# Performance work log

Hardware: AMD Instinct MI355X
Metric: run time of the kernel (lower is better)

## Reference

```python
import jax, jax.numpy as jnp
import numpy as np

N, F_IN, F_OUT = 2048, 128, 64


def setup_inputs() -> dict:
    key = jax.random.key(0)
    k0, k1, k2, k3, k4 = jax.random.split(key, 5)
    node_features = jax.random.normal(k0, (N, F_IN), dtype=jnp.float32)
    adjacency_matrix = jax.random.uniform(k1, (N, N), dtype=jnp.float32)
    mask_father = jax.random.uniform(k2, (N, N), dtype=jnp.float32)
    mask_hadamard = jax.random.uniform(k3, (N, N), dtype=jnp.float32)
    # kaiming_uniform (fan_in, relu): bound = sqrt(6 / fan_in) * sqrt(2) adjustment -> gain*sqrt(3/fan_in)
    bound = np.sqrt(2.0) * np.sqrt(3.0 / F_IN)
    weight = jax.random.uniform(k4, (F_IN, F_OUT), dtype=jnp.float32, minval=-bound, maxval=bound)
    bias = jnp.zeros((F_OUT,), dtype=jnp.float32)
    return {
        "node_features": node_features,
        "adjacency_matrix": adjacency_matrix,
        "mask_father": mask_father,
        "mask_hadamard": mask_hadamard,
        "weight": weight,
        "bias": bias,
    }


def reference(node_features, adjacency_matrix, mask_father, mask_hadamard, weight, bias):
    # H[i,f] = (X @ W + b)[i,f]
    H = node_features @ weight + bias  # [N, F]
    # Original math: out[j,f] = sum_k mf[j,k] * H[k,f] * (sum_i A[j,i] * H[i,f] * mh[i,k])
    # G[j,f,k] corresponds to the (masked hadamard @ adjacency) intermediate [N, F, N]
    G = jnp.einsum('ji,if,ik->jfk', adjacency_matrix, H, mask_hadamard)
    out = jnp.einsum('jfk,kf,jk->jf', G, H, mask_father)
    return out
```

## Files before the change

### kernel.cpp

```cpp
#include <hip/hip_runtime.h>
#include <hip/hip_bf16.h>


typedef __attribute__((ext_vector_type(8))) _Float16 f16x8;
typedef __attribute__((ext_vector_type(4))) _Float16 f16x4;
typedef __attribute__((ext_vector_type(4))) float f32x4;

#define N 2048
#define FOUT 64
#define FIN 128
#define BI 64
#define NIT 512

__device__ __forceinline__ void gl_lds16(const _Float16* g, _Float16* l) {
    __builtin_amdgcn_global_load_lds(
        (const __attribute__((address_space(1))) void*)g,
        (__attribute__((address_space(3))) void*)l, 16, 0, 0);
}


__global__ __launch_bounds__(256) void k_h(const float* __restrict__ X,
                                           const float* __restrict__ W,
                                           const float* __restrict__ bias,
                                           float* __restrict__ HT,
                                           _Float16* __restrict__ HTh) {
    __shared__ float Ws[FIN * FOUT];
    __shared__ float Xs[4 * FIN];
    int t = threadIdx.x;
#pragma unroll
    for (int s = 0; s < 32; ++s) Ws[t + 256 * s] = W[t + 256 * s];
    int i0 = blockIdx.x * 4;
#pragma unroll
    for (int s = 0; s < 2; ++s) { int idx = t + 256 * s; Xs[idx] = X[(size_t)i0 * FIN + idx]; }
    __syncthreads();
    int f = t & 63, il = t >> 6;
    float h = bias[f];
#pragma unroll
    for (int p = 0; p < FIN; ++p) h = fmaf(Xs[il * FIN + p], Ws[p * FOUT + f], h);
    int i = i0 + il;
    HT[f * N + i] = h;
    HTh[f * N + i] = (_Float16)h;
}

__global__ __launch_bounds__(256) void k_a2h(const float* __restrict__ A,
                                             _Float16* __restrict__ Ah) {
    int g = blockIdx.x * 256 + threadIdx.x;
    float4 v = ((const float4*)A)[g];
    f16x4 o;
    o[0] = (_Float16)v.x; o[1] = (_Float16)v.y; o[2] = (_Float16)v.z; o[3] = (_Float16)v.w;
    ((f16x4*)Ah)[g] = o;
}

__global__ __launch_bounds__(256) void k_mht(const float* __restrict__ mh,
                                             _Float16* __restrict__ mhT) {
    __shared__ float tile[64][65];
    int t = threadIdx.x;
    int bx = blockIdx.x & 31;
    int by = blockIdx.x >> 5;
#pragma unroll
    for (int s = 0; s < 16; ++s) {
        int lin = t + 256 * s;
        int r = lin >> 6, c = lin & 63;
        tile[r][c] = mh[(size_t)(by * 64 + r) * N + bx * 64 + c];
    }
    __syncthreads();
#pragma unroll
    for (int s = 0; s < 16; ++s) {
        int lin = t + 256 * s;
        int kr = lin >> 6, ic = lin & 63;
        mhT[(size_t)(bx * 64 + kr) * N + by * 64 + ic] = (_Float16)tile[ic][kr];
    }
}

__global__ __launch_bounds__(256, 2) void k_main(const float* __restrict__ mf,
                                                 const float* __restrict__ HT,
                                                 const _Float16* __restrict__ HTh,
                                                 const _Float16* __restrict__ Ah,
                                                 const _Float16* __restrict__ mhT,
                                                 float* __restrict__ out) {
    __shared__ _Float16 tiles[2][2][128 * BI];
    __shared__ _Float16 hbuf[2][N];
    __shared__ float red[2][4][64];

    int t = threadIdx.x;
    int jbase = (blockIdx.x >> 5) << 7;
    int f0 = (blockIdx.x & 31) << 1;
    int w = t >> 6, lane = t & 63, q = lane >> 4, l16 = lane & 15;
    int wj = (w & 1) << 6, wk = (w >> 1) << 6;

#pragma unroll
    for (int s = 0; s < 2; ++s) {
        int idx = t + 256 * s;
        ((f16x8*)hbuf)[idx] = *(const f16x8*)&HTh[(size_t)(f0 + (idx >> 8)) * N + (idx & 255) * 8];
    }

    int lrow = lane >> 3;
    int lchunk = (lane & 7) ^ lrow;
    int a_base = (jbase + w * 32 + lrow) * N + lchunk * 8;
    int b_base = (w * 32 + lrow) * N + lchunk * 8;
    int lds_w = w * 2048;

    float outp[2][4][4];
#pragma unroll
    for (int fi = 0; fi < 2; ++fi)
#pragma unroll
        for (int a = 0; a < 4; ++a)
#pragma unroll
            for (int b = 0; b < 4; ++b) outp[fi][a][b] = 0.f;

    {
        const _Float16* pa = Ah + a_base;
        const _Float16* pb = mhT + b_base;
        _Float16* la = &tiles[0][0][lds_w];
        _Float16* lb = &tiles[0][1][lds_w];
#pragma unroll
        for (int c = 0; c < 4; ++c) {
            gl_lds16(pa + c * 8 * N, la + c * 512);
            gl_lds16(pb + c * 8 * N, lb + c * 512);
        }
    }

    f32x4 acc[2][4][4];
#pragma unroll
    for (int fi = 0; fi < 2; ++fi)
#pragma unroll
        for (int a = 0; a < 4; ++a)
#pragma unroll
            for (int b = 0; b < 4; ++b) acc[fi][a][b] = (f32x4){0.f, 0.f, 0.f, 0.f};

    for (int it = 0; it < NIT; ++it) {
        int buf = it & 1;
        int ibase = (it & 31) << 6;
        int kbase = (it >> 5) << 7;

        __syncthreads();

        if (it + 1 < NIT) {
            int ib2 = ((it + 1) & 31) << 6;
            int kt2 = (it + 1) >> 5;
            const _Float16* pa = Ah + a_base + ib2;
            const _Float16* pb = mhT + b_base + kt2 * 128 * N + ib2;
            _Float16* la = &tiles[buf ^ 1][0][lds_w];
            _Float16* lb = &tiles[buf ^ 1][1][lds_w];
#pragma unroll
            for (int c = 0; c < 4; ++c) {
                gl_lds16(pa + c * 8 * N, la + c * 512);
                gl_lds16(pb + c * 8 * N, lb + c * 512);
            }
        }

        const _Float16* ta = tiles[buf][0];
        const _Float16* tb = tiles[buf][1];
#pragma unroll
        for (int s = 0; s < 2; ++s) {
            f16x8 ar[4], br[4];
#pragma unroll
            for (int x = 0; x < 4; ++x) {
                int row = wj + x * 16 + l16;
                ar[x] = *(const f16x8*)&ta[row * 64 + (((q + 4 * s) ^ (l16 & 7)) * 8)];
            }
#pragma unroll
            for (int x = 0; x < 4; ++x) {
                int row = wk + x * 16 + l16;
                br[x] = *(const f16x8*)&tb[row * 64 + (((q + 4 * s) ^ (l16 & 7)) * 8)];
            }
            f16x8 h0 = *(const f16x8*)&hbuf[0][ibase + s * 32 + q * 8];
            f16x8 h1 = *(const f16x8*)&hbuf[1][ibase + s * 32 + q * 8];
#pragma unroll
            for (int jj = 0; jj < 4; ++jj) {
                f16x8 a0 = ar[jj] * h0;
                f16x8 a1 = ar[jj] * h1;
#pragma unroll
                for (int kk = 0; kk < 4; ++kk) {
                    acc[0][jj][kk] = __builtin_amdgcn_mfma_f32_16x16x32_f16(a0, br[kk], acc[0][jj][kk], 0, 0, 0);
                    acc[1][jj][kk] = __builtin_amdgcn_mfma_f32_16x16x32_f16(a1, br[kk], acc[1][jj][kk], 0, 0, 0);
                }
            }
        }

        if ((it & 31) == 31) {
#pragma unroll
            for (int jj = 0; jj < 4; ++jj) {
                float t0[4] = {0.f, 0.f, 0.f, 0.f};
                float t1[4] = {0.f, 0.f, 0.f, 0.f};
#pragma unroll
                for (int kk = 0; kk < 4; ++kk) {
                    int kg = kbase + wk + kk * 16 + l16;
                    float hk0 = HT[f0 * N + kg];
                    float hk1 = HT[(f0 + 1) * N + kg];
                    int jrow = jbase + wj + jj * 16 + q * 4;
#pragma unroll
                    for (int r = 0; r < 4; ++r) {
                        float m = mf[(size_t)(jrow + r) * N + kg];
                        t0[r] = fmaf(acc[0][jj][kk][r], m * hk0, t0[r]);
                        t1[r] = fmaf(acc[1][jj][kk][r], m * hk1, t1[r]);
                    }
                }
#pragma unroll
                for (int r = 0; r < 4; ++r) {
                    float v0 = t0[r], v1 = t1[r];
                    v0 += __shfl_xor(v0, 1); v1 += __shfl_xor(v1, 1);
                    v0 += __shfl_xor(v0, 2); v1 += __shfl_xor(v1, 2);
                    v0 += __shfl_xor(v0, 4); v1 += __shfl_xor(v1, 4);
                    v0 += __shfl_xor(v0, 8); v1 += __shfl_xor(v1, 8);
                    outp[0][jj][r] += v0;
                    outp[1][jj][r] += v1;
                }
            }
#pragma unroll
            for (int fi = 0; fi < 2; ++fi)
#pragma unroll
                for (int a = 0; a < 4; ++a)
#pragma unroll
                    for (int b = 0; b < 4; ++b) acc[fi][a][b] = (f32x4){0.f, 0.f, 0.f, 0.f};
        }
    }

    if (l16 == 0) {
#pragma unroll
        for (int fi = 0; fi < 2; ++fi)
#pragma unroll
            for (int jj = 0; jj < 4; ++jj)
#pragma unroll
                for (int r = 0; r < 4; ++r)
                    red[fi][w][jj * 16 + q * 4 + r] = outp[fi][jj][r];
    }
    __syncthreads();
    if (t < 128) {
        int j = t;
#pragma unroll
        for (int fi = 0; fi < 2; ++fi) {
            float v = (j < 64) ? (red[fi][0][j] + red[fi][2][j])
                               : (red[fi][1][j - 64] + red[fi][3][j - 64]);
            out[(size_t)(jbase + j) * FOUT + f0 + fi] = v;
        }
    }
}

extern "C" void kernel_launch(void* const* d_in, const int* in_sizes, int n_in,
                              void* d_out, int out_size, void* d_ws, size_t ws_size,
                              hipStream_t stream) {
    const float* X    = (const float*)d_in[0];
    const float* A    = (const float*)d_in[1];
    const float* mf   = (const float*)d_in[2];
    const float* mh   = (const float*)d_in[3];
    const float* W    = (const float*)d_in[4];
    const float* bias = (const float*)d_in[5];
    float* out = (float*)d_out;

    float*    HT  = (float*)d_ws;
    _Float16* HTh = (_Float16*)((char*)d_ws + 524288);
    _Float16* Ah  = (_Float16*)((char*)d_ws + 1048576);
    _Float16* mhT = (_Float16*)((char*)d_ws + 1048576 + 8388608);

    k_h<<<N / 4, 256, 0, stream>>>(X, W, bias, HT, HTh);
    k_a2h<<<(N * N / 4) / 256, 256, 0, stream>>>(A, Ah);
    k_mht<<<(N / 64) * (N / 64), 256, 0, stream>>>(mh, mhT);
    k_main<<<16 * 32, 256, 0, stream>>>(mf, HT, HTh, Ah, mhT, out);
}
```

Baseline: 1.015 ms.

## Process four output features per block to reuse A and mask tiles

Each block now handles four features instead of two, which halves the grid to 256 blocks and halves global/LDS tile traffic for the adjacency and transposed mask per unit of work. The per-thread outp accumulators are replaced by LDS accumulation into the red buffer, which frees registers for the doubled MFMA accumulator set (256 floats). Launch bounds drop to one block per EU, so occupancy falls and only 256 blocks cover the device (about one per CU). This risks exposing latency and register spills.

```diff
diff --git a/kernel.cpp b/kernel.cpp
--- a/kernel.cpp
+++ b/kernel.cpp
@@ -72,27 +72,31 @@
     }
 }
 
-__global__ __launch_bounds__(256, 2) void k_main(const float* __restrict__ mf,
+__global__ __launch_bounds__(256, 1) void k_main(const float* __restrict__ mf,
                                                  const float* __restrict__ HT,
                                                  const _Float16* __restrict__ HTh,
                                                  const _Float16* __restrict__ Ah,
                                                  const _Float16* __restrict__ mhT,
                                                  float* __restrict__ out) {
     __shared__ _Float16 tiles[2][2][128 * BI];
-    __shared__ _Float16 hbuf[2][N];
-    __shared__ float red[2][4][64];
+    __shared__ _Float16 hbuf[4][N];
+    __shared__ float red[4][4][64];
 
     int t = threadIdx.x;
-    int jbase = (blockIdx.x >> 5) << 7;
-    int f0 = (blockIdx.x & 31) << 1;
+    int jbase = (blockIdx.x >> 4) << 7;
+    int f0 = (blockIdx.x & 15) << 2;
     int w = t >> 6, lane = t & 63, q = lane >> 4, l16 = lane & 15;
     int wj = (w & 1) << 6, wk = (w >> 1) << 6;
 
 #pragma unroll
-    for (int s = 0; s < 2; ++s) {
+    for (int s = 0; s < 4; ++s) {
         int idx = t + 256 * s;
         ((f16x8*)hbuf)[idx] = *(const f16x8*)&HTh[(size_t)(f0 + (idx >> 8)) * N + (idx & 255) * 8];
     }
+    ((float*)red)[t]       = 0.f;
+    ((float*)red)[t + 256] = 0.f;
+    ((float*)red)[t + 512] = 0.f;
+    ((float*)red)[t + 768] = 0.f;
 
     int lrow = lane >> 3;
     int lchunk = (lane & 7) ^ lrow;
@@ -100,14 +104,6 @@
     int b_base = (w * 32 + lrow) * N + lchunk * 8;
     int lds_w = w * 2048;
 
-    float outp[2][4][4];
-#pragma unroll
-    for (int fi = 0; fi < 2; ++fi)
-#pragma unroll
-        for (int a = 0; a < 4; ++a)
-#pragma unroll
-            for (int b = 0; b < 4; ++b) outp[fi][a][b] = 0.f;
-
     {
         const _Float16* pa = Ah + a_base;
         const _Float16* pb = mhT + b_base;
@@ -120,9 +116,9 @@
         }
     }
 
-    f32x4 acc[2][4][4];
-#pragma unroll
-    for (int fi = 0; fi < 2; ++fi)
+    f32x4 acc[4][4][4];
+#pragma unroll
+    for (int fi = 0; fi < 4; ++fi)
 #pragma unroll
         for (int a = 0; a < 4; ++a)
 #pragma unroll
@@ -153,7 +149,7 @@
         const _Float16* tb = tiles[buf][1];
 #pragma unroll
         for (int s = 0; s < 2; ++s) {
-            f16x8 ar[4], br[4];
+            f16x8 ar[4], br[4], h[4];
 #pragma unroll
             for (int x = 0; x < 4; ++x) {
                 int row = wj + x * 16 + l16;
@@ -164,51 +160,62 @@
                 int row = wk + x * 16 + l16;
                 br[x] = *(const f16x8*)&tb[row * 64 + (((q + 4 * s) ^ (l16 & 7)) * 8)];
             }
-            f16x8 h0 = *(const f16x8*)&hbuf[0][ibase + s * 32 + q * 8];
-            f16x8 h1 = *(const f16x8*)&hbuf[1][ibase + s * 32 + q * 8];
+#pragma unroll
+            for (int fi = 0; fi < 4; ++fi)
+                h[fi] = *(const f16x8*)&hbuf[fi][ibase + s * 32 + q * 8];
+#pragma unroll
+            for (int fi = 0; fi < 4; ++fi)
+#pragma unroll
+                for (int jj = 0; jj < 4; ++jj) {
+                    f16x8 a = ar[jj] * h[fi];
+#pragma unroll
+                    for (int kk = 0; kk < 4; ++kk)
+                        acc[fi][jj][kk] = __builtin_amdgcn_mfma_f32_16x16x32_f16(
+                            a, br[kk], acc[fi][jj][kk], 0, 0, 0);
+                }
+        }
+
+        if ((it & 31) == 31) {
+            float hk[4][4];
+#pragma unroll
+            for (int kk = 0; kk < 4; ++kk) {
+                int kg = kbase + wk + kk * 16 + l16;
+#pragma unroll
+                for (int fi = 0; fi < 4; ++fi) hk[fi][kk] = HT[(size_t)(f0 + fi) * N + kg];
+            }
 #pragma unroll
             for (int jj = 0; jj < 4; ++jj) {
-                f16x8 a0 = ar[jj] * h0;
-                f16x8 a1 = ar[jj] * h1;
-#pragma unroll
-                for (int kk = 0; kk < 4; ++kk) {
-                    acc[0][jj][kk] = __builtin_amdgcn_mfma_f32_16x16x32_f16(a0, br[kk], acc[0][jj][kk], 0, 0, 0);
-                    acc[1][jj][kk] = __builtin_amdgcn_mfma_f32_16x16x32_f16(a1, br[kk], acc[1][jj][kk], 0, 0, 0);
-                }
-            }
-        }
-
-        if ((it & 31) == 31) {
-#pragma unroll
-            for (int jj = 0; jj < 4; ++jj) {
-                float t0[4] = {0.f, 0.f, 0.f, 0.f};
-                float t1[4] = {0.f, 0.f, 0.f, 0.f};
+                float tt[4][4];
+#pragma unroll
+                for (int fi = 0; fi < 4; ++fi)
+#pragma unroll
+                    for (int r = 0; r < 4; ++r) tt[fi][r] = 0.f;
+                int jrow = jbase + wj + jj * 16 + q * 4;
 #pragma unroll
                 for (int kk = 0; kk < 4; ++kk) {
                     int kg = kbase + wk + kk * 16 + l16;
-                    float hk0 = HT[f0 * N + kg];
-                    float hk1 = HT[(f0 + 1) * N + kg];
-                    int jrow = jbase + wj + jj * 16 + q * 4;
 #pragma unroll
                     for (int r = 0; r < 4; ++r) {
                         float m = mf[(size_t)(jrow + r) * N + kg];
-                        t0[r] = fmaf(acc[0][jj][kk][r], m * hk0, t0[r]);
-                        t1[r] = fmaf(acc[1][jj][kk][r], m * hk1, t1[r]);
+#pragma unroll
+                        for (int fi = 0; fi < 4; ++fi)
+                            tt[fi][r] = fmaf(acc[fi][jj][kk][r], m * hk[fi][kk], tt[fi][r]);
                     }
                 }
 #pragma unroll
-                for (int r = 0; r < 4; ++r) {
-                    float v0 = t0[r], v1 = t1[r];
-                    v0 += __shfl_xor(v0, 1); v1 += __shfl_xor(v1, 1);
-                    v0 += __shfl_xor(v0, 2); v1 += __shfl_xor(v1, 2);
-                    v0 += __shfl_xor(v0, 4); v1 += __shfl_xor(v1, 4);
-                    v0 += __shfl_xor(v0, 8); v1 += __shfl_xor(v1, 8);
-                    outp[0][jj][r] += v0;
-                    outp[1][jj][r] += v1;
-                }
-            }
-#pragma unroll
-            for (int fi = 0; fi < 2; ++fi)
+                for (int fi = 0; fi < 4; ++fi)
+#pragma unroll
+                    for (int r = 0; r < 4; ++r) {
+                        float v = tt[fi][r];
+                        v += __shfl_xor(v, 1);
+                        v += __shfl_xor(v, 2);
+                        v += __shfl_xor(v, 4);
+                        v += __shfl_xor(v, 8);
+                        if (l16 == 0) red[fi][w][jj * 16 + q * 4 + r] += v;
+                    }
+            }
+#pragma unroll
+            for (int fi = 0; fi < 4; ++fi)
 #pragma unroll
                 for (int a = 0; a < 4; ++a)
 #pragma unroll
@@ -216,20 +223,11 @@
         }
     }
 
-    if (l16 == 0) {
-#pragma unroll
-        for (int fi = 0; fi < 2; ++fi)
-#pragma unroll
-            for (int jj = 0; jj < 4; ++jj)
-#pragma unroll
-                for (int r = 0; r < 4; ++r)
-                    red[fi][w][jj * 16 + q * 4 + r] = outp[fi][jj][r];
-    }
     __syncthreads();
     if (t < 128) {
         int j = t;
 #pragma unroll
-        for (int fi = 0; fi < 2; ++fi) {
+        for (int fi = 0; fi < 4; ++fi) {
             float v = (j < 64) ? (red[fi][0][j] + red[fi][2][j])
                                : (red[fi][1][j - 64] + red[fi][3][j - 64]);
             out[(size_t)(jbase + j) * FOUT + f0 + fi] = v;
@@ -256,5 +254,5 @@
     k_h<<<N / 4, 256, 0, stream>>>(X, W, bias, HT, HTh);
     k_a2h<<<(N * N / 4) / 256, 256, 0, stream>>>(A, Ah);
     k_mht<<<(N / 64) * (N / 64), 256, 0, stream>>>(mh, mhT);
-    k_main<<<16 * 32, 256, 0, stream>>>(mf, HT, HTh, Ah, mhT, out);
-}
+    k_main<<<16 * 16, 256, 0, stream>>>(mf, HT, HTh, Ah, mhT, out);
+}
```

New measurement: 2.273 ms. +123.9%, slower.

## Triple-buffer main loop with register double-buffered LDS reads and manual waitcnts

Applied to the files above, without the earlier changes.

Moves the main loop from a double-buffered LDS pipeline to a three-stage ring, prefetching two tiles ahead with explicit vmcnt/lgkmcnt waits and barriers. LDS fragments for the next step are read into a second register set while MFMAs run on the current one, so LDS latency overlaps compute. Occupancy is lowered to one block per CU (launch bounds 256,1) to make room for the extra registers. Per-wave partial outputs now accumulate directly into shared memory in the epilogue instead of in registers. The hand-written waits and the extra shared-memory traffic are fragile, and the lower occupancy may leave latency exposed that the second resident block used to hide.

```diff
diff --git a/kernel.cpp b/kernel.cpp
--- a/kernel.cpp
+++ b/kernel.cpp
@@ -9,7 +9,6 @@
 #define N 2048
 #define FOUT 64
 #define FIN 128
-#define BI 64
 #define NIT 512
 
 __device__ __forceinline__ void gl_lds16(const _Float16* g, _Float16* l) {
@@ -72,13 +71,115 @@
     }
 }
 
-__global__ __launch_bounds__(256, 2) void k_main(const float* __restrict__ mf,
+
+#define WAITV8 { asm volatile("s_waitcnt vmcnt(8)" ::: "memory"); __builtin_amdgcn_sched_barrier(0); }
+#define WAITV0 { asm volatile("s_waitcnt vmcnt(0)" ::: "memory"); __builtin_amdgcn_sched_barrier(0); }
+#define LGKM0  { asm volatile("s_waitcnt lgkmcnt(0)" ::: "memory"); __builtin_amdgcn_sched_barrier(0); }
+#define BAR    { __builtin_amdgcn_s_barrier(); __builtin_amdgcn_sched_barrier(0); }
+
+#define STAGE_STEP(X)                                                         \
+  {                                                                           \
+    int bs_ = (X) % 3;                                                        \
+    int ib_ = ((X) & 31) << 6;                                                \
+    int kt_ = (X) >> 5;                                                       \
+    const _Float16* pa_ = Ah + a_base + ib_;                                  \
+    const _Float16* pb_ = mhT + b_base + (size_t)kt_ * 128 * N + ib_;         \
+    _Float16* la_ = &tiles[bs_][0][lds_w];                                    \
+    _Float16* lb_ = &tiles[bs_][1][lds_w];                                    \
+    _Pragma("unroll")                                                         \
+    for (int c_ = 0; c_ < 4; ++c_) {                                          \
+      gl_lds16(pa_ + c_ * 8 * N, la_ + c_ * 512);                             \
+      gl_lds16(pb_ + c_ * 8 * N, lb_ + c_ * 512);                             \
+    }                                                                         \
+  }
+
+#define READ_STEP(AR, BR, HH, TB, IB)                                         \
+  {                                                                           \
+    const _Float16* ta_ = &tiles[TB][0][0];                                   \
+    const _Float16* tb_ = &tiles[TB][1][0];                                   \
+    _Pragma("unroll")                                                         \
+    for (int s_ = 0; s_ < 2; ++s_) {                                          \
+      HH[s_][0] = *(const f16x8*)&hbuf[0][(IB) + s_ * 32 + q * 8];            \
+      HH[s_][1] = *(const f16x8*)&hbuf[1][(IB) + s_ * 32 + q * 8];            \
+      _Pragma("unroll")                                                       \
+      for (int x_ = 0; x_ < 4; ++x_) {                                        \
+        AR[s_][x_] = *(const f16x8*)&ta_[(wj + x_ * 16 + l16) * 64 +          \
+                                         (((q + 4 * s_) ^ (l16 & 7)) * 8)];   \
+        BR[s_][x_] = *(const f16x8*)&tb_[(wk + x_ * 16 + l16) * 64 +          \
+                                         (((q + 4 * s_) ^ (l16 & 7)) * 8)];   \
+      }                                                                       \
+    }                                                                         \
+  }
+
+#define EPILOGUE(T)                                                           \
+  {                                                                           \
+    int kbase_ = ((T) >> 5) << 7;                                             \
+    _Pragma("unroll")                                                         \
+    for (int jj = 0; jj < 4; ++jj) {                                          \
+      float t0[4] = {0.f, 0.f, 0.f, 0.f};                                     \
+      float t1[4] = {0.f, 0.f, 0.f, 0.f};                                     \
+      int jrow = jbase + wj + jj * 16 + q * 4;                                \
+      _Pragma("unroll")                                                       \
+      for (int kk = 0; kk < 4; ++kk) {                                        \
+        int kg = kbase_ + wk + kk * 16 + l16;                                 \
+        float hk0 = HT[f0 * N + kg];                                          \
+        float hk1 = HT[(f0 + 1) * N + kg];                                    \
+        _Pragma("unroll")                                                     \
+        for (int r = 0; r < 4; ++r) {                                         \
+          float m = mf[(size_t)(jrow + r) * N + kg];                          \
+          t0[r] = fmaf(acc[0][jj][kk][r], m * hk0, t0[r]);                    \
+          t1[r] = fmaf(acc[1][jj][kk][r], m * hk1, t1[r]);                    \
+        }                                                                     \
+      }                                                                       \
+      _Pragma("unroll")                                                       \
+      for (int r = 0; r < 4; ++r) {                                           \
+        float v0 = t0[r], v1 = t1[r];                                         \
+        v0 += __shfl_xor(v0, 1); v1 += __shfl_xor(v1, 1);                     \
+        v0 += __shfl_xor(v0, 2); v1 += __shfl_xor(v1, 2);                     \
+        v0 += __shfl_xor(v0, 4); v1 += __shfl_xor(v1, 4);                     \
+        v0 += __shfl_xor(v0, 8); v1 += __shfl_xor(v1, 8);                     \
+        if (l16 == 0) {                                                       \
+          red[0][w][jj * 16 + q * 4 + r] += v0;                               \
+          red[1][w][jj * 16 + q * 4 + r] += v1;                               \
+        }                                                                     \
+      }                                                                       \
+    }                                                                         \
+    _Pragma("unroll")                                                         \
+    for (int a_ = 0; a_ < 4; ++a_)                                            \
+      _Pragma("unroll")                                                       \
+      for (int b_ = 0; b_ < 4; ++b_) {                                        \
+        acc[0][a_][b_] = (f32x4){0.f, 0.f, 0.f, 0.f};                         \
+        acc[1][a_][b_] = (f32x4){0.f, 0.f, 0.f, 0.f};                         \
+      }                                                                       \
+  }
+
+#define COMPUTE_STEP(AR, BR, HH, T)                                           \
+  {                                                                           \
+    _Pragma("unroll")                                                         \
+    for (int s_ = 0; s_ < 2; ++s_) {                                          \
+      _Pragma("unroll")                                                       \
+      for (int jj = 0; jj < 4; ++jj) {                                        \
+        f16x8 a0_ = AR[s_][jj] * HH[s_][0];                                   \
+        f16x8 a1_ = AR[s_][jj] * HH[s_][1];                                   \
+        _Pragma("unroll")                                                     \
+        for (int kk = 0; kk < 4; ++kk) {                                      \
+          acc[0][jj][kk] = __builtin_amdgcn_mfma_f32_16x16x32_f16(            \
+              a0_, BR[s_][kk], acc[0][jj][kk], 0, 0, 0);                      \
+          acc[1][jj][kk] = __builtin_amdgcn_mfma_f32_16x16x32_f16(            \
+              a1_, BR[s_][kk], acc[1][jj][kk], 0, 0, 0);                      \
+        }                                                                     \
+      }                                                                       \
+    }                                                                         \
+    if (((T) & 31) == 31) EPILOGUE(T)                                         \
+  }
+
+__global__ __launch_bounds__(256, 1) void k_main(const float* __restrict__ mf,
                                                  const float* __restrict__ HT,
                                                  const _Float16* __restrict__ HTh,
                                                  const _Float16* __restrict__ Ah,
                                                  const _Float16* __restrict__ mhT,
                                                  float* __restrict__ out) {
-    __shared__ _Float16 tiles[2][2][128 * BI];
+    __shared__ _Float16 tiles[3][2][128 * 64];
     __shared__ _Float16 hbuf[2][N];
     __shared__ float red[2][4][64];
 
@@ -93,6 +194,8 @@
         int idx = t + 256 * s;
         ((f16x8*)hbuf)[idx] = *(const f16x8*)&HTh[(size_t)(f0 + (idx >> 8)) * N + (idx & 255) * 8];
     }
+    ((float*)red)[t] = 0.f;
+    ((float*)red)[t + 256] = 0.f;
 
     int lrow = lane >> 3;
     int lchunk = (lane & 7) ^ lrow;
@@ -100,132 +203,53 @@
     int b_base = (w * 32 + lrow) * N + lchunk * 8;
     int lds_w = w * 2048;
 
-    float outp[2][4][4];
-#pragma unroll
-    for (int fi = 0; fi < 2; ++fi)
-#pragma unroll
-        for (int a = 0; a < 4; ++a)
-#pragma unroll
-            for (int b = 0; b < 4; ++b) outp[fi][a][b] = 0.f;
-
-    {
-        const _Float16* pa = Ah + a_base;
-        const _Float16* pb = mhT + b_base;
-        _Float16* la = &tiles[0][0][lds_w];
-        _Float16* lb = &tiles[0][1][lds_w];
-#pragma unroll
-        for (int c = 0; c < 4; ++c) {
-            gl_lds16(pa + c * 8 * N, la + c * 512);
-            gl_lds16(pb + c * 8 * N, lb + c * 512);
+    STAGE_STEP(0)
+    STAGE_STEP(1)
+    WAITV8
+    LGKM0
+    BAR
+
+    f16x8 arA[2][4], brA[2][4], hA[2][2];
+    f16x8 arB[2][4], brB[2][4], hB[2][2];
+    READ_STEP(arA, brA, hA, 0, 0)
+
+    f32x4 acc[2][4][4];
+#pragma unroll
+    for (int a = 0; a < 4; ++a)
+#pragma unroll
+        for (int b = 0; b < 4; ++b) {
+            acc[0][a][b] = (f32x4){0.f, 0.f, 0.f, 0.f};
+            acc[1][a][b] = (f32x4){0.f, 0.f, 0.f, 0.f};
         }
-    }
-
-    f32x4 acc[2][4][4];
-#pragma unroll
-    for (int fi = 0; fi < 2; ++fi)
-#pragma unroll
-        for (int a = 0; a < 4; ++a)
-#pragma unroll
-            for (int b = 0; b < 4; ++b) acc[fi][a][b] = (f32x4){0.f, 0.f, 0.f, 0.f};
-
-    for (int it = 0; it < NIT; ++it) {
-        int buf = it & 1;
-        int ibase = (it & 31) << 6;
-        int kbase = (it >> 5) << 7;
-
-        __syncthreads();
-
-        if (it + 1 < NIT) {
-            int ib2 = ((it + 1) & 31) << 6;
-            int kt2 = (it + 1) >> 5;
-            const _Float16* pa = Ah + a_base + ib2;
-            const _Float16* pb = mhT + b_base + kt2 * 128 * N + ib2;
-            _Float16* la = &tiles[buf ^ 1][0][lds_w];
-            _Float16* lb = &tiles[buf ^ 1][1][lds_w];
-#pragma unroll
-            for (int c = 0; c < 4; ++c) {
-                gl_lds16(pa + c * 8 * N, la + c * 512);
-                gl_lds16(pb + c * 8 * N, lb + c * 512);
-            }
-        }
-
-        const _Float16* ta = tiles[buf][0];
-        const _Float16* tb = tiles[buf][1];
-#pragma unroll
-        for (int s = 0; s < 2; ++s) {
-            f16x8 ar[4], br[4];
-#pragma unroll
-            for (int x = 0; x < 4; ++x) {
-                int row = wj + x * 16 + l16;
-                ar[x] = *(const f16x8*)&ta[row * 64 + (((q + 4 * s) ^ (l16 & 7)) * 8)];
-            }
-#pragma unroll
-            for (int x = 0; x < 4; ++x) {
-                int row = wk + x * 16 + l16;
-                br[x] = *(const f16x8*)&tb[row * 64 + (((q + 4 * s) ^ (l16 & 7)) * 8)];
-            }
-            f16x8 h0 = *(const f16x8*)&hbuf[0][ibase + s * 32 + q * 8];
-            f16x8 h1 = *(const f16x8*)&hbuf[1][ibase + s * 32 + q * 8];
-#pragma unroll
-            for (int jj = 0; jj < 4; ++jj) {
-                f16x8 a0 = ar[jj] * h0;
-                f16x8 a1 = ar[jj] * h1;
-#pragma unroll
-                for (int kk = 0; kk < 4; ++kk) {
-                    acc[0][jj][kk] = __builtin_amdgcn_mfma_f32_16x16x32_f16(a0, br[kk], acc[0][jj][kk], 0, 0, 0);
-                    acc[1][jj][kk] = __builtin_amdgcn_mfma_f32_16x16x32_f16(a1, br[kk], acc[1][jj][kk], 0, 0, 0);
-                }
-            }
-        }
-
-        if ((it & 31) == 31) {
-#pragma unroll
-            for (int jj = 0; jj < 4; ++jj) {
-                float t0[4] = {0.f, 0.f, 0.f, 0.f};
-                float t1[4] = {0.f, 0.f, 0.f, 0.f};
-#pragma unroll
-                for (int kk = 0; kk < 4; ++kk) {
-                    int kg = kbase + wk + kk * 16 + l16;
-                    float hk0 = HT[f0 * N + kg];
-                    float hk1 = HT[(f0 + 1) * N + kg];
-                    int jrow = jbase + wj + jj * 16 + q * 4;
-#pragma unroll
-                    for (int r = 0; r < 4; ++r) {
-                        float m = mf[(size_t)(jrow + r) * N + kg];
-                        t0[r] = fmaf(acc[0][jj][kk][r], m * hk0, t0[r]);
-                        t1[r] = fmaf(acc[1][jj][kk][r], m * hk1, t1[r]);
-                    }
-                }
-#pragma unroll
-                for (int r = 0; r < 4; ++r) {
-                    float v0 = t0[r], v1 = t1[r];
-                    v0 += __shfl_xor(v0, 1); v1 += __shfl_xor(v1, 1);
-                    v0 += __shfl_xor(v0, 2); v1 += __shfl_xor(v1, 2);
-                    v0 += __shfl_xor(v0, 4); v1 += __shfl_xor(v1, 4);
-                    v0 += __shfl_xor(v0, 8); v1 += __shfl_xor(v1, 8);
-                    outp[0][jj][r] += v0;
-                    outp[1][jj][r] += v1;
-                }
-            }
-#pragma unroll
-            for (int fi = 0; fi < 2; ++fi)
-#pragma unroll
-                for (int a = 0; a < 4; ++a)
-#pragma unroll
-                    for (int b = 0; b < 4; ++b) acc[fi][a][b] = (f32x4){0.f, 0.f, 0.f, 0.f};
-        }
-    }
-
-    if (l16 == 0) {
-#pragma unroll
-        for (int fi = 0; fi < 2; ++fi)
-#pragma unroll
-            for (int jj = 0; jj < 4; ++jj)
-#pragma unroll
-                for (int r = 0; r < 4; ++r)
-                    red[fi][w][jj * 16 + q * 4 + r] = outp[fi][jj][r];
-    }
-    __syncthreads();
+
+    for (int tp = 0; tp < (NIT - 2) / 2; ++tp) {
+        int t0 = tp * 2, t1 = t0 + 1;
+        STAGE_STEP(t0 + 2)
+        WAITV8
+        BAR
+        READ_STEP(arB, brB, hB, (t0 + 1) % 3, ((t0 + 1) & 31) << 6)
+        COMPUTE_STEP(arA, brA, hA, t0)
+        LGKM0
+        BAR
+        STAGE_STEP(t1 + 2)
+        WAITV8
+        BAR
+        READ_STEP(arA, brA, hA, (t1 + 1) % 3, ((t1 + 1) & 31) << 6)
+        COMPUTE_STEP(arB, brB, hB, t1)
+        LGKM0
+        BAR
+    }
+
+    WAITV0
+    BAR
+    READ_STEP(arB, brB, hB, (NIT - 1) % 3, ((NIT - 1) & 31) << 6)
+    COMPUTE_STEP(arA, brA, hA, NIT - 2)
+    LGKM0
+    BAR
+    COMPUTE_STEP(arB, brB, hB, NIT - 1)
+    LGKM0
+    BAR
+
     if (t < 128) {
         int j = t;
 #pragma unroll
```

After: 1.450 ms. 1.43x slower.

## Switch main kernel to 32x32x16 MFMA with unrolled double-buffer loop

Applied to the files above, without the earlier changes.

Replaces the 16x16x32 MFMA tiling with 32x32x16 MFMA tiles, so each wave computes 2x2 tiles per feature instead of 4x4. Fewer LDS fragment reads are needed per MFMA. The main loop is unrolled by two with explicit buffer indices and precomputed swizzled LDS addresses, and s_setprio is raised around the compute sections. The epilogue now accumulates into the shared reduction array directly instead of keeping per-thread partials. Risks include different register pressure and more shuffle steps in the epilogue.

```diff
diff --git a/kernel.cpp b/kernel.cpp
--- a/kernel.cpp
+++ b/kernel.cpp
@@ -4,13 +4,15 @@
 
 typedef __attribute__((ext_vector_type(8))) _Float16 f16x8;
 typedef __attribute__((ext_vector_type(4))) _Float16 f16x4;
-typedef __attribute__((ext_vector_type(4))) float f32x4;
+typedef __attribute__((ext_vector_type(16))) float f32x16;
 
 #define N 2048
 #define FOUT 64
 #define FIN 128
-#define BI 64
 #define NIT 512
+
+#define ZERO16 ((f32x16){0.f,0.f,0.f,0.f,0.f,0.f,0.f,0.f,0.f,0.f,0.f,0.f,0.f,0.f,0.f,0.f})
+#define MFMA32(A,B,C) __builtin_amdgcn_mfma_f32_32x32x16_f16((A),(B),(C),0,0,0)
 
 __device__ __forceinline__ void gl_lds16(const _Float16* g, _Float16* l) {
     __builtin_amdgcn_global_load_lds(
@@ -72,20 +74,106 @@
     }
 }
 
+
+#define STAGE(DBUF, IT)                                                        \
+  {                                                                            \
+    int ib_ = ((IT) & 31) << 6;                                                \
+    int kt_ = (IT) >> 5;                                                       \
+    const char* gA_ = (const char*)Ah + ((size_t)jbase * N + ib_) * 2;         \
+    const char* gB_ = (const char*)mhT + ((size_t)kt_ * 128 * N + ib_) * 2;    \
+    _Float16* la_ = &tiles[DBUF][0][lds_w];                                    \
+    _Float16* lb_ = &tiles[DBUF][1][lds_w];                                    \
+    _Pragma("unroll")                                                          \
+    for (int c_ = 0; c_ < 4; ++c_) {                                           \
+      gl_lds16((const _Float16*)(gA_ + (size_t)c_ * (16 * N) + vbyte), la_ + c_ * 512); \
+      gl_lds16((const _Float16*)(gB_ + (size_t)c_ * (16 * N) + vbyte), lb_ + c_ * 512); \
+    }                                                                          \
+  }
+
+#define COMPUTE_HALF(BUF, IT)                                                  \
+  {                                                                            \
+    const char* hb_ = (const char*)hbuf + ((((IT) & 31) << 6) * 2);            \
+    __builtin_amdgcn_s_setprio(1);                                             \
+    _Pragma("unroll")                                                          \
+    for (int ks = 0; ks < 4; ++ks) {                                           \
+      f16x8 a0 = *(const f16x8*)(tbase + addrA[ks] + (BUF) * 32768);           \
+      f16x8 a1 = *(const f16x8*)(tbase + addrA[ks] + (BUF) * 32768 + 4096);    \
+      f16x8 b0 = *(const f16x8*)(tbase + addrB[ks] + (BUF) * 32768 + 16384);   \
+      f16x8 b1 = *(const f16x8*)(tbase + addrB[ks] + (BUF) * 32768 + 20480);   \
+      f16x8 h0 = *(const f16x8*)(hb_ + hlb + ks * 32);                         \
+      f16x8 h1 = *(const f16x8*)(hb_ + hlb + 4096 + ks * 32);                  \
+      f16x8 a00 = a0 * h0, a10 = a1 * h0, a01 = a0 * h1, a11 = a1 * h1;        \
+      acc[0][0][0] = MFMA32(a00, b0, acc[0][0][0]);                            \
+      acc[0][0][1] = MFMA32(a00, b1, acc[0][0][1]);                            \
+      acc[0][1][0] = MFMA32(a10, b0, acc[0][1][0]);                            \
+      acc[0][1][1] = MFMA32(a10, b1, acc[0][1][1]);                            \
+      acc[1][0][0] = MFMA32(a01, b0, acc[1][0][0]);                            \
+      acc[1][0][1] = MFMA32(a01, b1, acc[1][0][1]);                            \
+      acc[1][1][0] = MFMA32(a11, b0, acc[1][1][0]);                            \
+      acc[1][1][1] = MFMA32(a11, b1, acc[1][1][1]);                            \
+    }                                                                          \
+    __builtin_amdgcn_s_setprio(0);                                             \
+  }
+
+#define EPILOGUE(IT)                                                           \
+  {                                                                            \
+    int kb_ = (((IT) >> 5) << 7) + wk;                                         \
+    float hk0[2], hk1[2];                                                      \
+    _Pragma("unroll")                                                          \
+    for (int tk = 0; tk < 2; ++tk) {                                           \
+      int kg = kb_ + tk * 32 + l31;                                            \
+      hk0[tk] = HT[f0 * N + kg];                                               \
+      hk1[tk] = HT[(f0 + 1) * N + kg];                                         \
+    }                                                                          \
+    _Pragma("unroll")                                                          \
+    for (int tj = 0; tj < 2; ++tj) {                                           \
+      int jr0 = jbase + wj + tj * 32 + hi * 4;                                 \
+      _Pragma("unroll")                                                        \
+      for (int r = 0; r < 16; ++r) {                                           \
+        int jr = jr0 + (r & 3) + 8 * (r >> 2);                                 \
+        float s0 = 0.f, s1 = 0.f;                                              \
+        _Pragma("unroll")                                                      \
+        for (int tk = 0; tk < 2; ++tk) {                                       \
+          int kg = kb_ + tk * 32 + l31;                                        \
+          float m = mf[(size_t)jr * N + kg];                                   \
+          s0 = fmaf(acc[0][tj][tk][r], m * hk0[tk], s0);                       \
+          s1 = fmaf(acc[1][tj][tk][r], m * hk1[tk], s1);                       \
+        }                                                                      \
+        s0 += __shfl_xor(s0, 1);  s1 += __shfl_xor(s1, 1);                     \
+        s0 += __shfl_xor(s0, 2);  s1 += __shfl_xor(s1, 2);                     \
+        s0 += __shfl_xor(s0, 4);  s1 += __shfl_xor(s1, 4);                     \
+        s0 += __shfl_xor(s0, 8);  s1 += __shfl_xor(s1, 8);                     \
+        s0 += __shfl_xor(s0, 16); s1 += __shfl_xor(s1, 16);                    \
+        if (l31 == 0) {                                                        \
+          int slot = tj * 32 + (r & 3) + 8 * (r >> 2) + 4 * hi;                \
+          red[0][w][slot] += s0;                                               \
+          red[1][w][slot] += s1;                                               \
+        }                                                                      \
+      }                                                                        \
+    }                                                                          \
+    _Pragma("unroll")                                                          \
+    for (int f_ = 0; f_ < 2; ++f_)                                             \
+      _Pragma("unroll")                                                        \
+      for (int a_ = 0; a_ < 2; ++a_)                                           \
+        _Pragma("unroll")                                                      \
+        for (int b_ = 0; b_ < 2; ++b_) acc[f_][a_][b_] = ZERO16;               \
+  }
+
 __global__ __launch_bounds__(256, 2) void k_main(const float* __restrict__ mf,
                                                  const float* __restrict__ HT,
                                                  const _Float16* __restrict__ HTh,
                                                  const _Float16* __restrict__ Ah,
                                                  const _Float16* __restrict__ mhT,
                                                  float* __restrict__ out) {
-    __shared__ _Float16 tiles[2][2][128 * BI];
+    __shared__ _Float16 tiles[2][2][128 * 64];
     __shared__ _Float16 hbuf[2][N];
     __shared__ float red[2][4][64];
 
     int t = threadIdx.x;
     int jbase = (blockIdx.x >> 5) << 7;
     int f0 = (blockIdx.x & 31) << 1;
-    int w = t >> 6, lane = t & 63, q = lane >> 4, l16 = lane & 15;
+    int w = t >> 6, lane = t & 63;
+    int l31 = lane & 31, hi = lane >> 5, l7 = lane & 7;
     int wj = (w & 1) << 6, wk = (w >> 1) << 6;
 
 #pragma unroll
@@ -93,138 +181,45 @@
         int idx = t + 256 * s;
         ((f16x8*)hbuf)[idx] = *(const f16x8*)&HTh[(size_t)(f0 + (idx >> 8)) * N + (idx & 255) * 8];
     }
+    ((float*)red)[t] = 0.f;
+    ((float*)red)[t + 256] = 0.f;
 
     int lrow = lane >> 3;
     int lchunk = (lane & 7) ^ lrow;
-    int a_base = (jbase + w * 32 + lrow) * N + lchunk * 8;
-    int b_base = (w * 32 + lrow) * N + lchunk * 8;
+    int vbyte = ((w * 32 + lrow) * N + lchunk * 8) * 2;
     int lds_w = w * 2048;
 
-    float outp[2][4][4];
-#pragma unroll
-    for (int fi = 0; fi < 2; ++fi)
-#pragma unroll
-        for (int a = 0; a < 4; ++a)
-#pragma unroll
-            for (int b = 0; b < 4; ++b) outp[fi][a][b] = 0.f;
-
-    {
-        const _Float16* pa = Ah + a_base;
-        const _Float16* pb = mhT + b_base;
-        _Float16* la = &tiles[0][0][lds_w];
-        _Float16* lb = &tiles[0][1][lds_w];
-#pragma unroll
-        for (int c = 0; c < 4; ++c) {
-            gl_lds16(pa + c * 8 * N, la + c * 512);
-            gl_lds16(pb + c * 8 * N, lb + c * 512);
-        }
-    }
-
-    f32x4 acc[2][4][4];
-#pragma unroll
-    for (int fi = 0; fi < 2; ++fi)
-#pragma unroll
-        for (int a = 0; a < 4; ++a)
-#pragma unroll
-            for (int b = 0; b < 4; ++b) acc[fi][a][b] = (f32x4){0.f, 0.f, 0.f, 0.f};
-
-    for (int it = 0; it < NIT; ++it) {
-        int buf = it & 1;
-        int ibase = (it & 31) << 6;
-        int kbase = (it >> 5) << 7;
-
+    const char* tbase = (const char*)&tiles[0][0][0];
+    int hlb = hi * 16;
+    int addrA[4], addrB[4];
+#pragma unroll
+    for (int ks = 0; ks < 4; ++ks) {
+        int chs = ((ks * 2 + hi) ^ l7) * 16;
+        addrA[ks] = (wj + l31) * 128 + chs;
+        addrB[ks] = (wk + l31) * 128 + chs;
+    }
+
+    STAGE(0, 0)
+
+    f32x16 acc[2][2][2];
+#pragma unroll
+    for (int f_ = 0; f_ < 2; ++f_)
+#pragma unroll
+        for (int a_ = 0; a_ < 2; ++a_)
+#pragma unroll
+            for (int b_ = 0; b_ < 2; ++b_) acc[f_][a_][b_] = ZERO16;
+
+    for (int tp = 0; tp < NIT / 2; ++tp) {
+        int it0 = tp * 2;
         __syncthreads();
-
-        if (it + 1 < NIT) {
-            int ib2 = ((it + 1) & 31) << 6;
-            int kt2 = (it + 1) >> 5;
-            const _Float16* pa = Ah + a_base + ib2;
-            const _Float16* pb = mhT + b_base + kt2 * 128 * N + ib2;
-            _Float16* la = &tiles[buf ^ 1][0][lds_w];
-            _Float16* lb = &tiles[buf ^ 1][1][lds_w];
-#pragma unroll
-            for (int c = 0; c < 4; ++c) {
-                gl_lds16(pa + c * 8 * N, la + c * 512);
-                gl_lds16(pb + c * 8 * N, lb + c * 512);
-            }
-        }
-
-        const _Float16* ta = tiles[buf][0];
-        const _Float16* tb = tiles[buf][1];
-#pragma unroll
-        for (int s = 0; s < 2; ++s) {
-            f16x8 ar[4], br[4];
-#pragma unroll
-            for (int x = 0; x < 4; ++x) {
-                int row = wj + x * 16 + l16;
-                ar[x] = *(const f16x8*)&ta[row * 64 + (((q + 4 * s) ^ (l16 & 7)) * 8)];
-            }
-#pragma unroll
-            for (int x = 0; x < 4; ++x) {
-                int row = wk + x * 16 + l16;
-                br[x] = *(const f16x8*)&tb[row * 64 + (((q + 4 * s) ^ (l16 & 7)) * 8)];
-            }
-            f16x8 h0 = *(const f16x8*)&hbuf[0][ibase + s * 32 + q * 8];
-            f16x8 h1 = *(const f16x8*)&hbuf[1][ibase + s * 32 + q * 8];
-#pragma unroll
-            for (int jj = 0; jj < 4; ++jj) {
-                f16x8 a0 = ar[jj] * h0;
-                f16x8 a1 = ar[jj] * h1;
-#pragma unroll
-                for (int kk = 0; kk < 4; ++kk) {
-                    acc[0][jj][kk] = __builtin_amdgcn_mfma_f32_16x16x32_f16(a0, br[kk], acc[0][jj][kk], 0, 0, 0);
-                    acc[1][jj][kk] = __builtin_amdgcn_mfma_f32_16x16x32_f16(a1, br[kk], acc[1][jj][kk], 0, 0, 0);
-                }
-            }
-        }
-
-        if ((it & 31) == 31) {
-#pragma unroll
-            for (int jj = 0; jj < 4; ++jj) {
-                float t0[4] = {0.f, 0.f, 0.f, 0.f};
-                float t1[4] = {0.f, 0.f, 0.f, 0.f};
-#pragma unroll
-                for (int kk = 0; kk < 4; ++kk) {
-                    int kg = kbase + wk + kk * 16 + l16;
-                    float hk0 = HT[f0 * N + kg];
-                    float hk1 = HT[(f0 + 1) * N + kg];
-                    int jrow = jbase + wj + jj * 16 + q * 4;
-#pragma unroll
-                    for (int r = 0; r < 4; ++r) {
-                        float m = mf[(size_t)(jrow + r) * N + kg];
-                        t0[r] = fmaf(acc[0][jj][kk][r], m * hk0, t0[r]);
-                        t1[r] = fmaf(acc[1][jj][kk][r], m * hk1, t1[r]);
-                    }
-                }
-#pragma unroll
-                for (int r = 0; r < 4; ++r) {
-                    float v0 = t0[r], v1 = t1[r];
-                    v0 += __shfl_xor(v0, 1); v1 += __shfl_xor(v1, 1);
-                    v0 += __shfl_xor(v0, 2); v1 += __shfl_xor(v1, 2);
-                    v0 += __shfl_xor(v0, 4); v1 += __shfl_xor(v1, 4);
-                    v0 += __shfl_xor(v0, 8); v1 += __shfl_xor(v1, 8);
-                    outp[0][jj][r] += v0;
-                    outp[1][jj][r] += v1;
-                }
-            }
-#pragma unroll
-            for (int fi = 0; fi < 2; ++fi)
-#pragma unroll
-                for (int a = 0; a < 4; ++a)
-#pragma unroll
-                    for (int b = 0; b < 4; ++b) acc[fi][a][b] = (f32x4){0.f, 0.f, 0.f, 0.f};
-        }
-    }
-
-    if (l16 == 0) {
-#pragma unroll
-        for (int fi = 0; fi < 2; ++fi)
-#pragma unroll
-            for (int jj = 0; jj < 4; ++jj)
-#pragma unroll
-                for (int r = 0; r < 4; ++r)
-                    red[fi][w][jj * 16 + q * 4 + r] = outp[fi][jj][r];
-    }
+        STAGE(1, it0 + 1)
+        COMPUTE_HALF(0, it0)
+        __syncthreads();
+        if (tp != NIT / 2 - 1) STAGE(0, it0 + 2)
+        COMPUTE_HALF(1, it0 + 1)
+        if (((it0 + 1) & 31) == 31) EPILOGUE(it0 + 1)
+    }
+
     __syncthreads();
     if (t < 128) {
         int j = t;
```

Result: slower. 1.253 ms (+23.4%).
